# Kernel tuning notes

Measured on AMD Instinct MI355X. Metric: run time of the kernel, lower is better.

The kernel has to match this reference:

```python
import jax, jax.numpy as jnp
import numpy as np

P = 10      # qubits
LQ = 4      # re-uploading layers
B = 4096    # batch
HID = 32    # readout hidden
DIM = 2 ** P


def _rz(t):
    t = jnp.asarray(t, jnp.float32)
    e = jnp.exp(-0.5j * t.astype(jnp.complex64))
    z = jnp.zeros_like(e)
    return jnp.stack([jnp.stack([e, z], -1), jnp.stack([z, jnp.conj(e)], -1)], -2)


def _rx(t):
    t = jnp.asarray(t, jnp.float32)
    c = jnp.cos(0.5 * t).astype(jnp.complex64)
    s = jnp.sin(0.5 * t).astype(jnp.complex64)
    return jnp.stack([jnp.stack([c, -1j * s], -1), jnp.stack([-1j * s, c], -1)], -2)


def _ry(t):
    t = jnp.asarray(t, jnp.float32)
    c = jnp.cos(0.5 * t).astype(jnp.complex64)
    s = jnp.sin(0.5 * t).astype(jnp.complex64)
    return jnp.stack([jnp.stack([c, -s], -1), jnp.stack([s, c], -1)], -2)


def _apply_1q(state, U, k):
    # state [B, 2^P] complex, U [B,2,2]; wire 0 = most-significant bit (PennyLane order)
    b = state.shape[0]
    s = state.reshape(b, 2 ** k, 2, -1)
    s = jnp.einsum('bij,bajc->baic', U, s)
    return s.reshape(b, -1)


def _apply_cnot(state, c, t):
    b = state.shape[0]
    a, d = min(c, t), max(c, t)
    s = state.reshape(b, 2 ** a, 2, 2 ** (d - a - 1), 2, -1)
    if c == a:  # control = smaller wire index (axis 2), target at axis 4
        hi = jnp.flip(s[:, :, 1], axis=3)  # [b,pre,mid,2,post] -> flip target bit
        s = jnp.stack([s[:, :, 0], hi], axis=2)
    else:       # control = larger wire index (axis 4), target at axis 2
        hi = jnp.flip(s[:, :, :, :, 1], axis=2)  # [b,pre,2,mid,post] -> flip target bit
        s = jnp.stack([s[:, :, :, :, 0], hi], axis=4)
    return s.reshape(b, -1)


def _meas_signs(p):
    # rows 0..p-1: Z_k signs; rows p..2p-1: Z_k Z_{(k+1)%p} signs
    idx = np.arange(2 ** p)
    bits = (idx[None, :] >> (p - 1 - np.arange(p)[:, None])) & 1
    z = (1.0 - 2.0 * bits).astype(np.float32)            # [p, 2^p]
    zz = z * np.roll(z, -1, axis=0)                      # [p, 2^p]
    return jnp.asarray(np.concatenate([z, zz], axis=0))  # [2p, 2^p]


MEAS = _meas_signs(P)


def _circuit_feats(theta, rot_weights, enc_scale, enc_bias):
    b = theta.shape[0]
    # Hadamard on every wire of |0...0> -> uniform superposition
    state = jnp.full((b, DIM), 1.0 / np.sqrt(DIM), dtype=jnp.complex64)
    for l in range(LQ):
        for k in range(P):
            t0 = enc_scale[l, k, 0] * theta[:, k] + enc_bias[l, k, 0]
            t1 = enc_scale[l, k, 1] * theta[:, k] + enc_bias[l, k, 1]
            U_enc = jnp.einsum('bij,bjk->bik', _rx(t1), _rz(t0))  # RX(t1) RZ(t0)
            w = rot_weights[l, k]
            # PennyLane Rot(phi,theta,omega) = RZ(omega) RY(theta) RZ(phi)
            U_rot = _rz(w[2]) @ _ry(w[1]) @ _rz(w[0])
            U = jnp.einsum('ij,bjk->bik', U_rot, U_enc)
            state = _apply_1q(state, U, k)
        for k in range(P):
            state = _apply_cnot(state, k, (k + 1) % P)
    probs = jnp.abs(state) ** 2              # [B, 2^P]
    return probs @ MEAS.T                    # [B, 2P] expectation values


def setup_inputs() -> dict:
    key = jax.random.key(0)
    ks = jax.random.split(key, 4)
    theta = jax.random.uniform(ks[0], (B, P), jnp.float32, -np.pi, np.pi)
    rot_weights = 0.02 * jax.random.normal(ks[1], (LQ, P, 3), dtype=jnp.float32)
    enc_scale = jnp.ones((LQ, P, 2), jnp.float32)   # clamp(0.5,1.5) of ones = ones
    enc_bias = jnp.zeros((LQ, P, 2), jnp.float32)
    n_meas = 2 * P
    W1 = jax.random.normal(ks[2], (HID, n_meas), dtype=jnp.float32) / np.sqrt(n_meas)
    b1 = jnp.zeros((HID,), jnp.float32)
    W2 = jax.random.normal(ks[3], (1, HID), dtype=jnp.float32) / np.sqrt(HID)
    b2 = jnp.zeros((1,), jnp.float32)
    return dict(theta=theta, rot_weights=rot_weights, enc_scale=enc_scale,
                enc_bias=enc_bias, W1=W1, b1=b1, W2=W2, b2=b2)


def reference(theta, rot_weights, enc_scale, enc_bias, W1, b1, W2, b2):
    feats = _circuit_feats(theta, rot_weights, enc_scale, enc_bias)
    h = jax.nn.silu(feats @ W1.T + b1)
    return (h @ W2.T + b2)[:, 0]  # [B]
```

## Files before the change

### kernel.cpp

```cpp
#include <hip/hip_runtime.h>
#include <math.h>

#define NQ   10
#define NLAY 4
#define BATCH 4096
#define HID  32
#define NM   20

typedef float f2 __attribute__((ext_vector_type(2)));

struct Tables {
    unsigned col[NLAY + 1][NQ];
    unsigned row[NLAY + 1][NQ];
};

constexpr Tables make_tables() {
    Tables t{};
    unsigned col[NQ] = {}, row[NQ] = {};
    for (int k = 0; k < NQ; ++k) { col[k] = 1u << (NQ - 1 - k); row[k] = 1u << (NQ - 1 - k); }
    for (int l = 0; l <= NLAY; ++l) {
        for (int k = 0; k < NQ; ++k) { t.col[l][k] = col[k]; t.row[l][k] = row[k]; }
        for (int k = 0; k < NQ; ++k) {
            int c = k, tg = (k + 1) % NQ;
            col[c] ^= col[tg];
            row[tg] ^= row[c];
        }
    }
    return t;
}

static constexpr Tables TB = make_tables();

__device__ __forceinline__ f2 mk2(float a, float b) { f2 r; r[0] = a; r[1] = b; return r; }
__device__ __forceinline__ f2 ffma(f2 a, f2 b, f2 c) { return __builtin_elementwise_fma(a, b, c); }

__device__ __forceinline__ f2 sh2(f2 a, int vl, int vs) {
    float lo = a[0], hi = a[1];
    if (vl) { lo = __shfl_xor(lo, vl); hi = __shfl_xor(hi, vl); }
    return vs ? mk2(hi, lo) : mk2(lo, hi);
}

__device__ __forceinline__ f2 apply_re(f2 ox, f2 oy, f2 px, f2 py,
                                       f2 ar, f2 ai, f2 br, f2 bi) {
    return ffma(ox, ar, ffma(-oy, ai, ffma(px, br, (-py) * bi)));
}
__device__ __forceinline__ f2 apply_im(f2 ox, f2 oy, f2 px, f2 py,
                                       f2 ar, f2 ai, f2 br, f2 bi) {
    return ffma(ox, ai, ffma(oy, ar, ffma(px, bi, py * br)));
}

__global__ __launch_bounds__(256, 4) void qrh_kernel(
    const float* __restrict__ theta, const float* __restrict__ rotw,
    const float* __restrict__ escale, const float* __restrict__ ebias,
    const float* __restrict__ W1, const float* __restrict__ b1,
    const float* __restrict__ W2, const float* __restrict__ b2,
    float* __restrict__ out)
{
    __shared__ float4 gmat[4][NLAY * NQ][2];

    const int tid  = threadIdx.x;
    const int lane = tid & 63;
    const int wv   = tid >> 6;
    const int b    = blockIdx.x * 4 + wv;

    if (lane < NLAY * NQ) {
        const int g = lane, l = g / NQ, k = g % NQ;
        const float th = theta[b * NQ + k];
        const int e2 = (l * NQ + k) * 2;
        const float t0 = escale[e2 + 0] * th + ebias[e2 + 0];
        const float t1 = escale[e2 + 1] * th + ebias[e2 + 1];
        float sn0, c0, sn1, c1;
        __sincosf(0.5f * t0, &sn0, &c0);
        __sincosf(0.5f * t1, &sn1, &c1);
        const f2 E00 = mk2( c1 * c0,  -c1 * sn0);
        const f2 E01 = mk2( sn1 * sn0, -sn1 * c0);
        const f2 E10 = mk2(-sn1 * sn0, -sn1 * c0);
        const f2 E11 = mk2( c1 * c0,   c1 * sn0);
        const int r3 = (l * NQ + k) * 3;
        const float w0 = rotw[r3 + 0], w1 = rotw[r3 + 1], w2 = rotw[r3 + 2];
        float cw, sw, ca0, sa0, ca1, sa1;
        __sincosf(0.5f * w1, &sw, &cw);
        __sincosf(0.5f * (w0 + w2), &sa0, &ca0);
        __sincosf(0.5f * (w0 - w2), &sa1, &ca1);
        const f2 R00 = mk2( cw * ca0, -cw * sa0);
        const f2 R01 = mk2(-sw * ca1, -sw * sa1);
        const f2 R10 = mk2( sw * ca1, -sw * sa1);
        const f2 R11 = mk2( cw * ca0,  cw * sa0);
        auto cm = [](f2 a, f2 bb) { return mk2(a[0]*bb[0] - a[1]*bb[1], a[0]*bb[1] + a[1]*bb[0]); };
        const f2 U00 = cm(R00, E00) + cm(R01, E10);
        const f2 U01 = cm(R00, E01) + cm(R01, E11);
        const f2 U10 = cm(R10, E00) + cm(R11, E10);
        const f2 U11 = cm(R10, E01) + cm(R11, E11);
        gmat[wv][g][0] = make_float4(U00[0], U00[1], U01[0], U01[1]);
        gmat[wv][g][1] = make_float4(U11[0], U11[1], U10[0], U10[1]);
    }
    __syncthreads();

    f2 sre[8], sim[8];
    #pragma unroll
    for (int r = 0; r < 8; ++r) { sre[r] = mk2(0.03125f, 0.03125f); sim[r] = mk2(0.f, 0.f); }

    #pragma unroll
    for (int l = 0; l < NLAY; ++l) {
        #pragma unroll
        for (int k = 0; k < NQ; ++k) {
            const unsigned v = TB.col[l][k];
            const unsigned m = TB.row[l][k];
            const int vl = (int)(v >> 4), vj = (int)(v & 15u);
            const int vr = vj >> 1, vs = vj & 1;
            const int ml = (int)(m >> 4), mj = (int)(m & 15u);
            const int mjr = mj >> 1, mjs = mj & 1;
            const int gi = l * NQ + k;

            const int laneP = ml ? (__popc((unsigned)lane & (unsigned)ml) & 1) : 0;
            const float4 A = gmat[wv][gi][laneP];
            f2 oc[2], pc[2];
            oc[0] = mk2(A.x, A.y); pc[0] = mk2(A.z, A.w);
            if (mj) {
                const float4 Bq = gmat[wv][gi][laneP ^ 1];
                oc[1] = mk2(Bq.x, Bq.y); pc[1] = mk2(Bq.z, Bq.w);
            } else { oc[1] = oc[0]; pc[1] = pc[0]; }

            f2 ocx[2], ocy[2], pcx[2], pcy[2];
            #pragma unroll
            for (int p_ = 0; p_ < 2; ++p_) {
                const int c0 = p_, c1 = p_ ^ mjs;
                ocx[p_] = mk2(oc[c0][0], oc[c1][0]);
                ocy[p_] = mk2(oc[c0][1], oc[c1][1]);
                pcx[p_] = mk2(pc[c0][0], pc[c1][0]);
                pcy[p_] = mk2(pc[c0][1], pc[c1][1]);
            }

            #pragma unroll
            for (int r = 0; r < 8; ++r) {
                const int r2 = r ^ vr;
                if (r2 < r) continue;
                const f2 pre_r = sh2(sre[r2], vl, vs);
                const f2 pim_r = sh2(sim[r2], vl, vs);
                const int pA = __builtin_popcount((unsigned)(r & mjr)) & 1;
                const f2 nre_r = apply_re(ocx[pA], ocy[pA], pcx[pA], pcy[pA],
                                          sre[r], sim[r], pre_r, pim_r);
                const f2 nim_r = apply_im(ocx[pA], ocy[pA], pcx[pA], pcy[pA],
                                          sre[r], sim[r], pre_r, pim_r);
                if (r2 != r) {
                    const f2 pre_2 = sh2(sre[r], vl, vs);
                    const f2 pim_2 = sh2(sim[r], vl, vs);
                    const int pB = __builtin_popcount((unsigned)(r2 & mjr)) & 1;
                    const f2 nre_2 = apply_re(ocx[pB], ocy[pB], pcx[pB], pcy[pB],
                                              sre[r2], sim[r2], pre_2, pim_2);
                    const f2 nim_2 = apply_im(ocx[pB], ocy[pB], pcx[pB], pcy[pB],
                                              sre[r2], sim[r2], pre_2, pim_2);
                    sre[r2] = nre_2; sim[r2] = nim_2;
                }
                sre[r] = nre_r; sim[r] = nim_r;
            }
        }
    }

    float w[16];
    #pragma unroll
    for (int r = 0; r < 8; ++r) {
        const f2 p2 = ffma(sre[r], sre[r], sim[r] * sim[r]);
        w[2 * r] = p2[0]; w[2 * r + 1] = p2[1];
    }
    #pragma unroll
    for (int bit = 1; bit < 16; bit <<= 1) {
        #pragma unroll
        for (int j = 0; j < 16; ++j) {
            if (!(j & bit)) {
                const float a = w[j], c = w[j | bit];
                w[j] = a + c; w[j | bit] = a - c;
            }
        }
    }

    float feats[NM];
    #pragma unroll
    for (int f = 0; f < NM; ++f) {
        const unsigned M = (f < NQ) ? TB.row[NLAY][f]
                                    : (TB.row[NLAY][f - NQ] ^ TB.row[NLAY][(f - NQ + 1) % NQ]);
        const int Ml = (int)(M >> 4), Mj = (int)(M & 15u);
        const float s = w[Mj];
        const int lsgn = __popc((unsigned)lane & (unsigned)Ml) & 1;
        feats[f] = lsgn ? -s : s;
    }
    #pragma unroll
    for (int sh = 1; sh < 64; sh <<= 1) {
        #pragma unroll
        for (int f = 0; f < NM; ++f) feats[f] += __shfl_xor(feats[f], sh);
    }

    float part = 0.f;
    if (lane < HID) {
        float acc = b1[lane];
        #pragma unroll
        for (int mm = 0; mm < NM; ++mm) acc = fmaf(feats[mm], W1[lane * NM + mm], acc);
        const float sg = 1.f / (1.f + __expf(-acc));
        part = acc * sg * W2[lane];
    }
    #pragma unroll
    for (int sh = 32; sh >= 1; sh >>= 1) part += __shfl_xor(part, sh);
    if (lane == 0) out[b] = part + b2[0];
}

extern "C" void kernel_launch(void* const* d_in, const int* in_sizes, int n_in,
                              void* d_out, int out_size, void* d_ws, size_t ws_size,
                              hipStream_t stream) {
    (void)in_sizes; (void)n_in; (void)out_size; (void)d_ws; (void)ws_size;
    const float* theta = (const float*)d_in[0];
    const float* rotw  = (const float*)d_in[1];
    const float* esc   = (const float*)d_in[2];
    const float* ebi   = (const float*)d_in[3];
    const float* W1    = (const float*)d_in[4];
    const float* b1    = (const float*)d_in[5];
    const float* W2    = (const float*)d_in[6];
    const float* b2    = (const float*)d_in[7];
    float* out = (float*)d_out;

    qrh_kernel<<<BATCH / 4, 256, 0, stream>>>(theta, rotw, esc, ebi, W1, b1, W2, b2, out);
}
```

Before: 111.7 us.

## Split each batch element's statevector across two wavefronts with LDS exchange

After: 130.1 us. 1.16x slower.

```diff
diff --git a/kernel.cpp b/kernel.cpp
--- a/kernel.cpp
+++ b/kernel.cpp
@@ -33,6 +33,7 @@
 
 __device__ __forceinline__ f2 mk2(float a, float b) { f2 r; r[0] = a; r[1] = b; return r; }
 __device__ __forceinline__ f2 ffma(f2 a, f2 b, f2 c) { return __builtin_elementwise_fma(a, b, c); }
+__device__ __forceinline__ f2 swap2(f2 a) { return mk2(a[1], a[0]); }
 
 __device__ __forceinline__ f2 sh2(f2 a, int vl, int vs) {
     float lo = a[0], hi = a[1];
@@ -49,22 +50,25 @@
     return ffma(ox, ai, ffma(oy, ar, ffma(px, bi, py * br)));
 }
 
-__global__ __launch_bounds__(256, 4) void qrh_kernel(
+__global__ __launch_bounds__(128, 8) void qrh_kernel(
     const float* __restrict__ theta, const float* __restrict__ rotw,
     const float* __restrict__ escale, const float* __restrict__ ebias,
     const float* __restrict__ W1, const float* __restrict__ b1,
     const float* __restrict__ W2, const float* __restrict__ b2,
     float* __restrict__ out)
 {
-    __shared__ float4 gmat[4][NLAY * NQ][2];
+    __shared__ float4 gmat[NLAY * NQ][2];
+    __shared__ f2 xbuf[2][4][128];
+    __shared__ float fbuf[NM];
 
     const int tid  = threadIdx.x;
     const int lane = tid & 63;
-    const int wv   = tid >> 6;
-    const int b    = blockIdx.x * 4 + wv;
-
-    if (lane < NLAY * NQ) {
-        const int g = lane, l = g / NQ, k = g % NQ;
+    const int wv9  = tid >> 6;
+    const int sUp  = tid;
+    const int b    = blockIdx.x;
+
+    if (tid < NLAY * NQ) {
+        const int g = tid, l = g / NQ, k = g % NQ;
         const float th = theta[b * NQ + k];
         const int e2 = (l * NQ + k) * 2;
         const float t0 = escale[e2 + 0] * th + ebias[e2 + 0];
@@ -91,14 +95,14 @@
         const f2 U01 = cm(R00, E01) + cm(R01, E11);
         const f2 U10 = cm(R10, E00) + cm(R11, E10);
         const f2 U11 = cm(R10, E01) + cm(R11, E11);
-        gmat[wv][g][0] = make_float4(U00[0], U00[1], U01[0], U01[1]);
-        gmat[wv][g][1] = make_float4(U11[0], U11[1], U10[0], U10[1]);
+        gmat[g][0] = make_float4(U00[0], U00[1], U01[0], U01[1]);
+        gmat[g][1] = make_float4(U11[0], U11[1], U10[0], U10[1]);
     }
     __syncthreads();
 
-    f2 sre[8], sim[8];
-    #pragma unroll
-    for (int r = 0; r < 8; ++r) { sre[r] = mk2(0.03125f, 0.03125f); sim[r] = mk2(0.f, 0.f); }
+    f2 sre[4], sim[4];
+    #pragma unroll
+    for (int r = 0; r < 4; ++r) { sre[r] = mk2(0.03125f, 0.03125f); sim[r] = mk2(0.f, 0.f); }
 
     #pragma unroll
     for (int l = 0; l < NLAY; ++l) {
@@ -106,21 +110,19 @@
         for (int k = 0; k < NQ; ++k) {
             const unsigned v = TB.col[l][k];
             const unsigned m = TB.row[l][k];
-            const int vl = (int)(v >> 4), vj = (int)(v & 15u);
-            const int vr = vj >> 1, vs = vj & 1;
-            const int ml = (int)(m >> 4), mj = (int)(m & 15u);
-            const int mjr = mj >> 1, mjs = mj & 1;
+            const int vw = (int)(v >> 9) & 1;
+            const int dUp = (int)(v >> 3) & 127;
+            const int vlane = dUp & 63;
+            const int vj = (int)(v & 7u), vr = vj >> 1, vs = vj & 1;
+            const unsigned mUp = m >> 3;
+            const int mj = (int)(m & 7u), mjr = mj >> 1, mjs = mj & 1;
             const int gi = l * NQ + k;
 
-            const int laneP = ml ? (__popc((unsigned)lane & (unsigned)ml) & 1) : 0;
-            const float4 A = gmat[wv][gi][laneP];
-            f2 oc[2], pc[2];
-            oc[0] = mk2(A.x, A.y); pc[0] = mk2(A.z, A.w);
-            if (mj) {
-                const float4 Bq = gmat[wv][gi][laneP ^ 1];
-                oc[1] = mk2(Bq.x, Bq.y); pc[1] = mk2(Bq.z, Bq.w);
-            } else { oc[1] = oc[0]; pc[1] = pc[0]; }
-
+            const int laneP = mUp ? (__popc((unsigned)sUp & mUp) & 1) : 0;
+            const float4 A  = gmat[gi][laneP];
+            const float4 Bq = gmat[gi][laneP ^ 1];
+            f2 oc[2] = { mk2(A.x, A.y), mk2(Bq.x, Bq.y) };
+            f2 pc[2] = { mk2(A.z, A.w), mk2(Bq.z, Bq.w) };
             f2 ocx[2], ocy[2], pcx[2], pcy[2];
             #pragma unroll
             for (int p_ = 0; p_ < 2; ++p_) {
@@ -131,42 +133,56 @@
                 pcy[p_] = mk2(pc[c0][1], pc[c1][1]);
             }
 
+            f2 pre[4], pim[4];
+            if (vw) {
+                #pragma unroll
+                for (int r = 0; r < 4; ++r) { xbuf[0][r][sUp] = sre[r]; xbuf[1][r][sUp] = sim[r]; }
+                __syncthreads();
+                const int pUp = sUp ^ dUp;
+                #pragma unroll
+                for (int r = 0; r < 4; ++r) {
+                    const f2 qre = xbuf[0][r ^ vr][pUp];
+                    const f2 qim = xbuf[1][r ^ vr][pUp];
+                    pre[r] = vs ? swap2(qre) : qre;
+                    pim[r] = vs ? swap2(qim) : qim;
+                }
+                __syncthreads();
+            } else if (vlane) {
+                #pragma unroll
+                for (int r = 0; r < 4; ++r) {
+                    pre[r] = sh2(sre[r ^ vr], vlane, vs);
+                    pim[r] = sh2(sim[r ^ vr], vlane, vs);
+                }
+            } else {
+                #pragma unroll
+                for (int r = 0; r < 4; ++r) {
+                    pre[r] = vs ? swap2(sre[r ^ vr]) : sre[r ^ vr];
+                    pim[r] = vs ? swap2(sim[r ^ vr]) : sim[r ^ vr];
+                }
+            }
+
             #pragma unroll
-            for (int r = 0; r < 8; ++r) {
-                const int r2 = r ^ vr;
-                if (r2 < r) continue;
-                const f2 pre_r = sh2(sre[r2], vl, vs);
-                const f2 pim_r = sh2(sim[r2], vl, vs);
-                const int pA = __builtin_popcount((unsigned)(r & mjr)) & 1;
-                const f2 nre_r = apply_re(ocx[pA], ocy[pA], pcx[pA], pcy[pA],
-                                          sre[r], sim[r], pre_r, pim_r);
-                const f2 nim_r = apply_im(ocx[pA], ocy[pA], pcx[pA], pcy[pA],
-                                          sre[r], sim[r], pre_r, pim_r);
-                if (r2 != r) {
-                    const f2 pre_2 = sh2(sre[r], vl, vs);
-                    const f2 pim_2 = sh2(sim[r], vl, vs);
-                    const int pB = __builtin_popcount((unsigned)(r2 & mjr)) & 1;
-                    const f2 nre_2 = apply_re(ocx[pB], ocy[pB], pcx[pB], pcy[pB],
-                                              sre[r2], sim[r2], pre_2, pim_2);
-                    const f2 nim_2 = apply_im(ocx[pB], ocy[pB], pcx[pB], pcy[pB],
-                                              sre[r2], sim[r2], pre_2, pim_2);
-                    sre[r2] = nre_2; sim[r2] = nim_2;
-                }
-                sre[r] = nre_r; sim[r] = nim_r;
-            }
-        }
-    }
-
-    float w[16];
-    #pragma unroll
-    for (int r = 0; r < 8; ++r) {
+            for (int r = 0; r < 4; ++r) {
+                const int p_ = __builtin_popcount((unsigned)(r & mjr)) & 1;
+                const f2 nre = apply_re(ocx[p_], ocy[p_], pcx[p_], pcy[p_],
+                                        sre[r], sim[r], pre[r], pim[r]);
+                const f2 nim = apply_im(ocx[p_], ocy[p_], pcx[p_], pcy[p_],
+                                        sre[r], sim[r], pre[r], pim[r]);
+                sre[r] = nre; sim[r] = nim;
+            }
+        }
+    }
+
+    float w[8];
+    #pragma unroll
+    for (int r = 0; r < 4; ++r) {
         const f2 p2 = ffma(sre[r], sre[r], sim[r] * sim[r]);
         w[2 * r] = p2[0]; w[2 * r + 1] = p2[1];
     }
     #pragma unroll
-    for (int bit = 1; bit < 16; bit <<= 1) {
-        #pragma unroll
-        for (int j = 0; j < 16; ++j) {
+    for (int bit = 1; bit < 8; bit <<= 1) {
+        #pragma unroll
+        for (int j = 0; j < 8; ++j) {
             if (!(j & bit)) {
                 const float a = w[j], c = w[j | bit];
                 w[j] = a + c; w[j | bit] = a - c;
@@ -179,9 +195,10 @@
     for (int f = 0; f < NM; ++f) {
         const unsigned M = (f < NQ) ? TB.row[NLAY][f]
                                     : (TB.row[NLAY][f - NQ] ^ TB.row[NLAY][(f - NQ + 1) % NQ]);
-        const int Ml = (int)(M >> 4), Mj = (int)(M & 15u);
+        const unsigned MUp = M >> 3;
+        const int Mj = (int)(M & 7u);
         const float s = w[Mj];
-        const int lsgn = __popc((unsigned)lane & (unsigned)Ml) & 1;
+        const int lsgn = __popc((unsigned)sUp & MUp) & 1;
         feats[f] = lsgn ? -s : s;
     }
     #pragma unroll
@@ -190,17 +207,26 @@
         for (int f = 0; f < NM; ++f) feats[f] += __shfl_xor(feats[f], sh);
     }
 
-    float part = 0.f;
-    if (lane < HID) {
-        float acc = b1[lane];
-        #pragma unroll
-        for (int mm = 0; mm < NM; ++mm) acc = fmaf(feats[mm], W1[lane * NM + mm], acc);
-        const float sg = 1.f / (1.f + __expf(-acc));
-        part = acc * sg * W2[lane];
-    }
-    #pragma unroll
-    for (int sh = 32; sh >= 1; sh >>= 1) part += __shfl_xor(part, sh);
-    if (lane == 0) out[b] = part + b2[0];
+    if (wv9 == 1 && lane == 0) {
+        #pragma unroll
+        for (int f = 0; f < NM; ++f) fbuf[f] = feats[f];
+    }
+    __syncthreads();
+    if (wv9 == 0) {
+        #pragma unroll
+        for (int f = 0; f < NM; ++f) feats[f] += fbuf[f];
+        float part = 0.f;
+        if (lane < HID) {
+            float acc = b1[lane];
+            #pragma unroll
+            for (int mm = 0; mm < NM; ++mm) acc = fmaf(feats[mm], W1[lane * NM + mm], acc);
+            const float sg = 1.f / (1.f + __expf(-acc));
+            part = acc * sg * W2[lane];
+        }
+        #pragma unroll
+        for (int sh = 32; sh >= 1; sh >>= 1) part += __shfl_xor(part, sh);
+        if (lane == 0) out[b] = part + b2[0];
+    }
 }
 
 extern "C" void kernel_launch(void* const* d_in, const int* in_sizes, int n_in,
@@ -217,5 +243,5 @@
     const float* b2    = (const float*)d_in[7];
     float* out = (float*)d_out;
 
-    qrh_kernel<<<BATCH / 4, 256, 0, stream>>>(theta, rotw, esc, ebi, W1, b1, W2, b2, out);
-}
+    qrh_kernel<<<BATCH, 128, 0, stream>>>(theta, rotw, esc, ebi, W1, b1, W2, b2, out);
+}
```
